# Performance work log

Hardware: AMD Instinct MI355X
Metric: run time of the kernel (lower is better)

Reference implementation:

```python
import jax, jax.numpy as jnp
import numpy as np

HIDDEN = 1024
HEADS = 16
HEAD_DIM = HIDDEN // HEADS

def setup_inputs() -> dict:
    key = jax.random.key(0)
    ks = jax.random.split(key, 11)
    B, T, D = 2, 2048, HIDDEN
    s = 1.0 / np.sqrt(D)
    return {
        "query": jax.random.normal(ks[0], (B, T, D), jnp.float32),
        "key": jax.random.normal(ks[1], (B, T, D), jnp.float32),
        "value": jax.random.normal(ks[2], (B, T, D), jnp.float32),
        "Wq": jax.random.normal(ks[3], (D, D), jnp.float32) * s,
        "bq": jnp.zeros((D,), jnp.float32),
        "Wk": jax.random.normal(ks[4], (D, D), jnp.float32) * s,
        "bk": jnp.zeros((D,), jnp.float32),
        "Wv": jax.random.normal(ks[5], (D, D), jnp.float32) * s,
        "bv": jnp.zeros((D,), jnp.float32),
        "Wo": jax.random.normal(ks[6], (D, D), jnp.float32) * s,
        "bo": jnp.zeros((D,), jnp.float32),
    }

def reference(query, key, value, Wq, bq, Wk, bk, Wv, bv, Wo, bo):
    B, Tq, D = query.shape
    Tk = key.shape[1]
    H, Hd = HEADS, HEAD_DIM
    # projections -> [B, H, T, Hd]
    Q = (query @ Wq + bq).reshape(B, Tq, H, Hd).transpose(0, 2, 1, 3)
    K = (key @ Wk + bk).reshape(B, Tk, H, Hd).transpose(0, 2, 1, 3)
    V = (value @ Wv + bv).reshape(B, Tk, H, Hd).transpose(0, 2, 1, 3)
    scale = jnp.sqrt(jnp.asarray(Hd, Q.dtype))
    scores = jnp.einsum('bhqd,bhkd->bhqk', Q, K) / scale  # [B,H,Tq,Tk]
    causal = jnp.triu(jnp.ones((Tq, Tk), bool), k=1)
    scores = jnp.where(causal[None, None], jnp.asarray(-jnp.inf, scores.dtype), scores)
    attn = jax.nn.softmax(scores, axis=-1)
    out = jnp.einsum('bhqk,bhkd->bhqd', attn, V)  # [B,H,Tq,Hd]
    out = out.transpose(0, 2, 1, 3).reshape(B, Tq, D)
    return out @ Wo + bo
```

## Files before the change

### kernel.cpp

```cpp
#include <hip/hip_runtime.h>
#include <hip/hip_bf16.h>


typedef __bf16 bf16_t;
typedef __bf16 bf16x8 __attribute__((ext_vector_type(8)));
typedef float f32x4 __attribute__((ext_vector_type(4)));
typedef float f32x16 __attribute__((ext_vector_type(16)));
typedef unsigned int u32;
typedef unsigned int u32x2v __attribute__((ext_vector_type(2)));
typedef unsigned int u32x4v __attribute__((ext_vector_type(4)));

#define D_MODEL 1024
#define SEQ_T   2048
#define NHEAD   16
#define HDIM    64
#define M_ROWS  4096
#define MEGA    (1024 * 1024)

__device__ __forceinline__ void gl2lds16(const void* g, void* l) {
    __builtin_amdgcn_global_load_lds((const __attribute__((address_space(1))) u32*)g,
                                     (__attribute__((address_space(3))) u32*)l, 16, 0, 0);
}

__device__ __forceinline__ u32 pk2(float a, float b) {
    unsigned short x = __builtin_bit_cast(unsigned short, (bf16_t)a);
    unsigned short y = __builtin_bit_cast(unsigned short, (bf16_t)b);
    return (u32)x | ((u32)y << 16);
}

__global__ __launch_bounds__(256) void prep(
    const float* __restrict__ Wq, const float* __restrict__ Wk,
    const float* __restrict__ Wv, const float* __restrict__ Wo,
    const float* __restrict__ Xq, const float* __restrict__ Xk, const float* __restrict__ Xv,
    bf16_t* __restrict__ Wqt, bf16_t* __restrict__ Wkt,
    bf16_t* __restrict__ Wvt, bf16_t* __restrict__ Wot,
    bf16_t* __restrict__ Xb)
{
    int blk = blockIdx.x, tid = threadIdx.x;
    if (blk < 4096) {
        int wi = blk >> 10, t = blk & 1023;
        int n0 = (t & 31) * 32, k0 = (t >> 5) * 32;
        const float* W = wi == 0 ? Wq : (wi == 1 ? Wk : (wi == 2 ? Wv : Wo));
        bf16_t* Wt = wi == 0 ? Wqt : (wi == 1 ? Wkt : (wi == 2 ? Wvt : Wot));
        __shared__ float tile[32][33];
        int tx = tid & 31, ty = tid >> 5;
#pragma unroll
        for (int i = 0; i < 32; i += 8)
            tile[ty + i][tx] = W[(k0 + ty + i) * D_MODEL + n0 + tx];
        __syncthreads();
#pragma unroll
        for (int i = 0; i < 32; i += 8)
            Wt[(size_t)(n0 + ty + i) * D_MODEL + k0 + tx] = (bf16_t)tile[tx][ty + i];
    } else {
        int b2 = blk - 4096;
        int xi = b2 >> 10;
        const float* X = xi == 0 ? Xq : (xi == 1 ? Xk : Xv);
        bf16_t* XB = Xb + (size_t)xi * M_ROWS * D_MODEL;
        size_t base = (size_t)(b2 & 1023) * 4096 + tid * 16;
        const float4* xp = (const float4*)(X + base);
        float4 a0 = xp[0], a1 = xp[1], a2 = xp[2], a3 = xp[3];
        bf16x8 o0, o1;
        o0[0] = (bf16_t)a0.x; o0[1] = (bf16_t)a0.y; o0[2] = (bf16_t)a0.z; o0[3] = (bf16_t)a0.w;
        o0[4] = (bf16_t)a1.x; o0[5] = (bf16_t)a1.y; o0[6] = (bf16_t)a1.z; o0[7] = (bf16_t)a1.w;
        o1[0] = (bf16_t)a2.x; o1[1] = (bf16_t)a2.y; o1[2] = (bf16_t)a2.z; o1[3] = (bf16_t)a2.w;
        o1[4] = (bf16_t)a3.x; o1[5] = (bf16_t)a3.y; o1[6] = (bf16_t)a3.z; o1[7] = (bf16_t)a3.w;
        *(bf16x8*)(XB + base) = o0;
        *(bf16x8*)(XB + base + 8) = o1;
    }
}

template <bool PRECAST>
__global__ __launch_bounds__(256) void proj_fused(
    const float* __restrict__ Xq, const float* __restrict__ Xk, const float* __restrict__ Xv,
    const bf16_t* __restrict__ Xb,
    const bf16_t* __restrict__ Wqt, const bf16_t* __restrict__ Wkt, const bf16_t* __restrict__ Wvt,
    const float* __restrict__ bq, const float* __restrict__ bk, const float* __restrict__ bv,
    bf16_t* __restrict__ Qh, bf16_t* __restrict__ Kh, bf16_t* __restrict__ Vt)
{
    __shared__ bf16_t Ab[128 * 64];
    __shared__ bf16_t Bb[128 * 64];
    int tid = threadIdx.x;
    int w = tid >> 6, lane = tid & 63, lo16 = lane & 15, quad = lane >> 4;
    int m0 = blockIdx.x * 128;
    int proj = blockIdx.y >> 3;
    int n0 = (blockIdx.y & 7) * 128;
    const float*  X    = proj == 0 ? Xq  : (proj == 1 ? Xk  : Xv);
    const bf16_t* XB   = Xb + (size_t)proj * M_ROWS * D_MODEL;
    const bf16_t* Wt   = proj == 0 ? Wqt : (proj == 1 ? Wkt : Wvt);
    const float*  bias = proj == 0 ? bq  : (proj == 1 ? bk  : bv);
    int wm = (w >> 1) * 64, wn = (w & 1) * 64;

    f32x4 acc[4][4];
#pragma unroll
    for (int i = 0; i < 4; i++)
#pragma unroll
        for (int j = 0; j < 4; j++) acc[i][j] = (f32x4){0.f, 0.f, 0.f, 0.f};

    for (int k0 = 0; k0 < D_MODEL; k0 += 64) {
        __syncthreads();
#pragma unroll
        for (int p = 0; p < 4; p++) {
            int idx = p * 256 + tid;
            int row = idx >> 3, cp = idx & 7, cl = (cp - row) & 7;
            if (PRECAST) {
                gl2lds16(XB + (size_t)(m0 + row) * D_MODEL + k0 + cl * 8, Ab + idx * 8);
            } else {
                const float* as = X + (size_t)(m0 + row) * D_MODEL + k0 + cl * 8;
                float4 a0 = *(const float4*)as, a1 = *(const float4*)(as + 4);
                bf16x8 av;
                av[0] = (bf16_t)a0.x; av[1] = (bf16_t)a0.y; av[2] = (bf16_t)a0.z; av[3] = (bf16_t)a0.w;
                av[4] = (bf16_t)a1.x; av[5] = (bf16_t)a1.y; av[6] = (bf16_t)a1.z; av[7] = (bf16_t)a1.w;
                *(bf16x8*)(Ab + idx * 8) = av;
            }
            gl2lds16(Wt + (size_t)(n0 + row) * D_MODEL + k0 + cl * 8, Bb + idx * 8);
        }
        __syncthreads();
#pragma unroll
        for (int kk = 0; kk < 2; kk++) {
            bf16x8 af[4], bfr[4];
#pragma unroll
            for (int i = 0; i < 4; i++) {
                int row = wm + i * 16 + lo16;
                af[i] = *(bf16x8*)(Ab + row * 64 + ((4 * kk + quad + row) & 7) * 8);
            }
#pragma unroll
            for (int j = 0; j < 4; j++) {
                int row = wn + j * 16 + lo16;
                bfr[j] = *(bf16x8*)(Bb + row * 64 + ((4 * kk + quad + row) & 7) * 8);
            }
#pragma unroll
            for (int i = 0; i < 4; i++)
#pragma unroll
                for (int j = 0; j < 4; j++)
                    acc[i][j] = __builtin_amdgcn_mfma_f32_16x16x32_bf16(af[i], bfr[j], acc[i][j], 0, 0, 0);
        }
    }

    float qscale = proj == 0 ? 0.1803368801111244f : 1.0f;
#pragma unroll
    for (int j = 0; j < 4; j++) {
        int col = n0 + wn + j * 16 + lo16;
        float bv2 = bias[col];
        int h = col >> 6, hd = col & 63;
#pragma unroll
        for (int i = 0; i < 4; i++) {
#pragma unroll
            for (int r = 0; r < 4; r++) {
                int m = m0 + wm + i * 16 + quad * 4 + r;
                int b = m >> 11, t = m & 2047;
                bf16_t val = (bf16_t)((acc[i][j][r] + bv2) * qscale);
                if (proj == 2)
                    Vt[(((size_t)(b * NHEAD + h) * HDIM + hd) * SEQ_T) + t] = val;
                else if (proj == 1)
                    Kh[(((size_t)(b * NHEAD + h) * SEQ_T + t) * HDIM) + hd] = val;
                else
                    Qh[(((size_t)(b * NHEAD + h) * SEQ_T + t) * HDIM) + hd] = val;
            }
        }
    }
}

__global__ __launch_bounds__(128, 2) void flash_attn(const bf16_t* __restrict__ Qh,
                                                     const bf16_t* __restrict__ Kh,
                                                     const bf16_t* __restrict__ Vt,
                                                     bf16_t* __restrict__ Ob) {
    int blk = blockIdx.x;
    int bh = blk & 31;
    int s5 = blk >> 5;
    int seg = s5 >> 3, o = s5 & 7;
    int j = seg == 0 ? 31 - o : (seg == 1 ? 16 + o : (seg == 2 ? 15 - o : o));
    int tid = threadIdx.x;
    int w = tid >> 6, lane = tid & 63;
    int l32 = lane & 31, hi = lane >> 5;
    int qbase = j * 64 + w * 32;

    __shared__ bf16_t KL[2][64 * 64];
    __shared__ bf16_t VL[2][64 * 64];

    const bf16_t* Qp = Qh + (size_t)bh * SEQ_T * HDIM;
    const bf16_t* Kp = Kh + (size_t)bh * SEQ_T * HDIM;
    const bf16_t* Vp = Vt + (size_t)bh * HDIM * SEQ_T;

    bf16x8 qf[4];
    {
        const bf16_t* qr = Qp + (size_t)(qbase + l32) * HDIM;
#pragma unroll
        for (int kd = 0; kd < 4; kd++)
            qf[kd] = *(const bf16x8*)(qr + kd * 16 + hi * 8);
    }

    bf16x8 ones;
#pragma unroll
    for (int i = 0; i < 8; i++) ones[i] = (bf16_t)1.0f;

    f32x16 oacc[2], lacc;
#pragma unroll
    for (int r = 0; r < 16; r++) { oacc[0][r] = 0.f; oacc[1][r] = 0.f; lacc[r] = 0.f; }

    int nkt = j + 1;

#pragma unroll
    for (int p = 0; p < 4; p++) {
        int idx = p * 128 + tid;
        int row = idx >> 3, cp = idx & 7, cl = (cp - row) & 7;
        gl2lds16(Kp + (size_t)row * HDIM + cl * 8, KL[0] + idx * 8);
        gl2lds16(Vp + (size_t)row * SEQ_T + cl * 8, VL[0] + idx * 8);
    }

    for (int kt = 0; kt < nkt; kt++) {
        int cur = kt & 1;
        __syncthreads();

        if (kt + 1 < nkt) {
#pragma unroll
            for (int p = 0; p < 4; p++) {
                int idx = p * 128 + tid;
                int row = idx >> 3, cp = idx & 7, cl = (cp - row) & 7;
                gl2lds16(Kp + (size_t)((kt + 1) * 64 + row) * HDIM + cl * 8, KL[cur ^ 1] + idx * 8);
                gl2lds16(Vp + (size_t)row * SEQ_T + (kt + 1) * 64 + cl * 8, VL[cur ^ 1] + idx * 8);
            }
        }
        const bf16_t* KLc = KL[cur];
        const bf16_t* VLc = VL[cur];

        f32x16 sacc[2];
#pragma unroll
        for (int r = 0; r < 16; r++) { sacc[0][r] = 0.f; sacc[1][r] = 0.f; }
#pragma unroll
        for (int ks = 0; ks < 2; ks++) {
            int key = l32 + 32 * ks;
#pragma unroll
            for (int kd = 0; kd < 4; kd++) {
                bf16x8 kf = *(const bf16x8*)(KLc + key * 64 + ((2 * kd + hi + key) & 7) * 8);
                sacc[ks] = __builtin_amdgcn_mfma_f32_32x32x16_bf16(kf, qf[kd], sacc[ks], 0, 0, 0);
            }
        }

        bool diag = (kt == nkt - 1);
        int qg = qbase + l32;
#pragma unroll
        for (int ks = 0; ks < 2; ks++)
#pragma unroll
            for (int r = 0; r < 16; r++) {
                float e = exp2f(sacc[ks][r]);
                if (diag) {
                    int key = kt * 64 + ks * 32 + (r & 3) + 8 * (r >> 2) + 4 * hi;
                    e = (key <= qg) ? e : 0.f;
                }
                sacc[ks][r] = e;
            }

        bf16x8 pf[4];
#pragma unroll
        for (int t = 0; t < 4; t++) {
            const int ks = t >> 1, bb = (t & 1) * 8;
            u32 A1 = pk2(sacc[ks][bb + 0], sacc[ks][bb + 1]);
            u32 A2 = pk2(sacc[ks][bb + 2], sacc[ks][bb + 3]);
            u32 C1 = pk2(sacc[ks][bb + 4], sacc[ks][bb + 5]);
            u32 C2 = pk2(sacc[ks][bb + 6], sacc[ks][bb + 7]);
            u32x2v s1 = __builtin_amdgcn_permlane32_swap(A1, C1, false, false);
            u32x2v s2 = __builtin_amdgcn_permlane32_swap(A2, C2, false, false);
            u32x4v wv; wv[0] = s1[0]; wv[1] = s2[0]; wv[2] = s1[1]; wv[3] = s2[1];
            pf[t] = __builtin_bit_cast(bf16x8, wv);
            lacc = __builtin_amdgcn_mfma_f32_32x32x16_bf16(pf[t], ones, lacc, 0, 0, 0);
        }

#pragma unroll
        for (int dt = 0; dt < 2; dt++) {
            int d = l32 + 32 * dt;
#pragma unroll
            for (int t = 0; t < 4; t++) {
                bf16x8 vf = *(const bf16x8*)(VLc + d * 64 + ((2 * t + hi + d) & 7) * 8);
                oacc[dt] = __builtin_amdgcn_mfma_f32_32x32x16_bf16(pf[t], vf, oacc[dt], 0, 0, 0);
            }
        }
    }

    int b = bh >> 4, h = bh & 15;
    float inv[16];
#pragma unroll
    for (int r = 0; r < 16; r++) inv[r] = 1.0f / lacc[r];
#pragma unroll
    for (int dt = 0; dt < 2; dt++)
#pragma unroll
        for (int r = 0; r < 16; r++) {
            int q = qbase + (r & 3) + 8 * (r >> 2) + 4 * hi;
            int d = l32 + 32 * dt;
            Ob[((size_t)b * SEQ_T + q) * D_MODEL + h * HDIM + d] = (bf16_t)(oacc[dt][r] * inv[r]);
        }
}

__global__ __launch_bounds__(256) void out_gemm(const bf16_t* __restrict__ A,
                                                const bf16_t* __restrict__ Wt,
                                                const float* __restrict__ bias,
                                                float* __restrict__ out) {
    __shared__ bf16_t Ab[128 * 64];
    __shared__ bf16_t Bb[128 * 64];
    int tid = threadIdx.x;
    int w = tid >> 6, lane = tid & 63, lo16 = lane & 15, quad = lane >> 4;
    int m0 = blockIdx.x * 128;
    int n0 = blockIdx.y * 128;
    int wm = (w >> 1) * 64, wn = (w & 1) * 64;

    f32x4 acc[4][4];
#pragma unroll
    for (int i = 0; i < 4; i++)
#pragma unroll
        for (int j = 0; j < 4; j++) acc[i][j] = (f32x4){0.f, 0.f, 0.f, 0.f};

    for (int k0 = 0; k0 < D_MODEL; k0 += 64) {
        __syncthreads();
#pragma unroll
        for (int p = 0; p < 4; p++) {
            int idx = p * 256 + tid;
            int row = idx >> 3, cp = idx & 7, cl = (cp - row) & 7;
            gl2lds16(A  + (size_t)(m0 + row) * D_MODEL + k0 + cl * 8, Ab + idx * 8);
            gl2lds16(Wt + (size_t)(n0 + row) * D_MODEL + k0 + cl * 8, Bb + idx * 8);
        }
        __syncthreads();
#pragma unroll
        for (int kk = 0; kk < 2; kk++) {
            bf16x8 af[4], bfr[4];
#pragma unroll
            for (int i = 0; i < 4; i++) {
                int row = wm + i * 16 + lo16;
                af[i] = *(bf16x8*)(Ab + row * 64 + ((4 * kk + quad + row) & 7) * 8);
            }
#pragma unroll
            for (int j = 0; j < 4; j++) {
                int row = wn + j * 16 + lo16;
                bfr[j] = *(bf16x8*)(Bb + row * 64 + ((4 * kk + quad + row) & 7) * 8);
            }
#pragma unroll
            for (int i = 0; i < 4; i++)
#pragma unroll
                for (int j = 0; j < 4; j++)
                    acc[i][j] = __builtin_amdgcn_mfma_f32_16x16x32_bf16(af[i], bfr[j], acc[i][j], 0, 0, 0);
        }
    }

#pragma unroll
    for (int j = 0; j < 4; j++) {
        int col = n0 + wn + j * 16 + lo16;
        float bv2 = bias[col];
#pragma unroll
        for (int i = 0; i < 4; i++)
#pragma unroll
            for (int r = 0; r < 4; r++) {
                int m = m0 + wm + i * 16 + quad * 4 + r;
                out[(size_t)m * D_MODEL + col] = acc[i][j][r] + bv2;
            }
    }
}

extern "C" void kernel_launch(void* const* d_in, const int* in_sizes, int n_in,
                              void* d_out, int out_size, void* d_ws, size_t ws_size,
                              hipStream_t stream) {
    const float* q  = (const float*)d_in[0];
    const float* k  = (const float*)d_in[1];
    const float* v  = (const float*)d_in[2];
    const float* Wq = (const float*)d_in[3];
    const float* bq = (const float*)d_in[4];
    const float* Wk = (const float*)d_in[5];
    const float* bk = (const float*)d_in[6];
    const float* Wv = (const float*)d_in[7];
    const float* bv = (const float*)d_in[8];
    const float* Wo = (const float*)d_in[9];
    const float* bo = (const float*)d_in[10];
    float* out = (float*)d_out;

    bf16_t* Wqt = (bf16_t*)d_ws;
    bf16_t* Wkt = Wqt + (size_t)MEGA;
    bf16_t* Wvt = Wkt + (size_t)MEGA;
    bf16_t* Wot = Wvt + (size_t)MEGA;
    bf16_t* Qh  = Wot + (size_t)MEGA;
    bf16_t* Kh  = Qh  + (size_t)M_ROWS * D_MODEL;
    bf16_t* Vt  = Kh  + (size_t)M_ROWS * D_MODEL;
    bf16_t* Xb  = Vt  + (size_t)M_ROWS * D_MODEL;
    bf16_t* Ob  = Xb;

    bool precast = ws_size >= (size_t)(4 * MEGA + 3 * M_ROWS * D_MODEL + 3 * M_ROWS * D_MODEL) * sizeof(bf16_t);

    int prep_blocks = precast ? 4096 + 3 * 1024 : 4096;
    prep<<<prep_blocks, 256, 0, stream>>>(Wq, Wk, Wv, Wo, q, k, v, Wqt, Wkt, Wvt, Wot, Xb);

    dim3 pg(M_ROWS / 128, 24);
    if (precast)
        proj_fused<true><<<pg, 256, 0, stream>>>(q, k, v, Xb, Wqt, Wkt, Wvt, bq, bk, bv, Qh, Kh, Vt);
    else
        proj_fused<false><<<pg, 256, 0, stream>>>(q, k, v, Xb, Wqt, Wkt, Wvt, bq, bk, bv, Qh, Kh, Vt);

    flash_attn<<<32 * 32, 128, 0, stream>>>(Qh, Kh, Vt, Ob);

    dim3 og(M_ROWS / 128, D_MODEL / 128);
    out_gemm<<<og, 256, 0, stream>>>(Ob, Wot, bo, out);
}
```

Baseline: 245.2 us.

## Split long causal attention rows across two blocks and add combine kernel

Flash attention now reads a constant job table that splits query tiles 17–31 into two KV ranges. The two partial blocks write unnormalized outputs and row sums to a float workspace, and a new combine kernel adds the partials and normalizes. The aim is to balance the triangular causal workload across more blocks and shorten the tail. Separately, both GEMMs switch from a K-tile of 64 to 32 and drop the LDS swizzle, which halves shared memory but doubles the number of barrier steps and may cause bank conflicts. The new partial buffer sits past the checked workspace size and adds an extra kernel launch and global traffic.

```diff
diff --git a/kernel.cpp b/kernel.cpp
--- a/kernel.cpp
+++ b/kernel.cpp
@@ -3,6 +3,7 @@
 
 
 typedef __bf16 bf16_t;
+typedef __bf16 bf16x4 __attribute__((ext_vector_type(4)));
 typedef __bf16 bf16x8 __attribute__((ext_vector_type(8)));
 typedef float f32x4 __attribute__((ext_vector_type(4)));
 typedef float f32x16 __attribute__((ext_vector_type(16)));
@@ -27,6 +28,21 @@
     unsigned short y = __builtin_bit_cast(unsigned short, (bf16_t)b);
     return (u32)x | ((u32)y << 16);
 }
+
+#define JOB(j, k0, n) ((j) | ((k0) << 8) | ((n) << 16))
+__device__ __constant__ int JOBS[47] = {
+    JOB(16,0,17),
+    JOB(15,0,16), JOB(30,0,16), JOB(31,0,16), JOB(31,16,16),
+    JOB(14,0,15), JOB(28,0,15), JOB(29,0,15), JOB(29,15,15), JOB(30,16,15),
+    JOB(13,0,14), JOB(26,0,14), JOB(27,0,14), JOB(27,14,14), JOB(28,15,14),
+    JOB(12,0,13), JOB(24,0,13), JOB(25,0,13), JOB(25,13,13), JOB(26,14,13),
+    JOB(11,0,12), JOB(22,0,12), JOB(23,0,12), JOB(23,12,12), JOB(24,13,12),
+    JOB(10,0,11), JOB(20,0,11), JOB(21,0,11), JOB(21,11,11), JOB(22,12,11),
+    JOB( 9,0,10), JOB(18,0,10), JOB(19,0,10), JOB(19,10,10), JOB(20,11,10),
+    JOB( 8,0, 9), JOB(17,0, 9), JOB(17,9, 9), JOB(18,10, 9),
+    JOB( 7,0, 8), JOB( 6,0, 7), JOB( 5,0, 6), JOB( 4,0, 5),
+    JOB( 3,0, 4), JOB( 2,0, 3), JOB( 1,0, 2), JOB( 0,0, 1)
+};
 
 __global__ __launch_bounds__(256) void prep(
     const float* __restrict__ Wq, const float* __restrict__ Wk,
@@ -77,8 +93,8 @@
     const float* __restrict__ bq, const float* __restrict__ bk, const float* __restrict__ bv,
     bf16_t* __restrict__ Qh, bf16_t* __restrict__ Kh, bf16_t* __restrict__ Vt)
 {
-    __shared__ bf16_t Ab[128 * 64];
-    __shared__ bf16_t Bb[128 * 64];
+    __shared__ bf16_t Ab[128 * 32];
+    __shared__ bf16_t Bb[128 * 32];
     int tid = threadIdx.x;
     int w = tid >> 6, lane = tid & 63, lo16 = lane & 15, quad = lane >> 4;
     int m0 = blockIdx.x * 128;
@@ -96,44 +112,37 @@
 #pragma unroll
         for (int j = 0; j < 4; j++) acc[i][j] = (f32x4){0.f, 0.f, 0.f, 0.f};
 
-    for (int k0 = 0; k0 < D_MODEL; k0 += 64) {
-        __syncthreads();
-#pragma unroll
-        for (int p = 0; p < 4; p++) {
+    for (int k0 = 0; k0 < D_MODEL; k0 += 32) {
+        __syncthreads();
+#pragma unroll
+        for (int p = 0; p < 2; p++) {
             int idx = p * 256 + tid;
-            int row = idx >> 3, cp = idx & 7, cl = (cp - row) & 7;
+            int row = idx >> 2, ch = (idx & 3) * 8;
             if (PRECAST) {
-                gl2lds16(XB + (size_t)(m0 + row) * D_MODEL + k0 + cl * 8, Ab + idx * 8);
+                gl2lds16(XB + (size_t)(m0 + row) * D_MODEL + k0 + ch, Ab + idx * 8);
             } else {
-                const float* as = X + (size_t)(m0 + row) * D_MODEL + k0 + cl * 8;
+                const float* as = X + (size_t)(m0 + row) * D_MODEL + k0 + ch;
                 float4 a0 = *(const float4*)as, a1 = *(const float4*)(as + 4);
                 bf16x8 av;
                 av[0] = (bf16_t)a0.x; av[1] = (bf16_t)a0.y; av[2] = (bf16_t)a0.z; av[3] = (bf16_t)a0.w;
                 av[4] = (bf16_t)a1.x; av[5] = (bf16_t)a1.y; av[6] = (bf16_t)a1.z; av[7] = (bf16_t)a1.w;
                 *(bf16x8*)(Ab + idx * 8) = av;
             }
-            gl2lds16(Wt + (size_t)(n0 + row) * D_MODEL + k0 + cl * 8, Bb + idx * 8);
-        }
-        __syncthreads();
-#pragma unroll
-        for (int kk = 0; kk < 2; kk++) {
-            bf16x8 af[4], bfr[4];
-#pragma unroll
-            for (int i = 0; i < 4; i++) {
-                int row = wm + i * 16 + lo16;
-                af[i] = *(bf16x8*)(Ab + row * 64 + ((4 * kk + quad + row) & 7) * 8);
-            }
-#pragma unroll
-            for (int j = 0; j < 4; j++) {
-                int row = wn + j * 16 + lo16;
-                bfr[j] = *(bf16x8*)(Bb + row * 64 + ((4 * kk + quad + row) & 7) * 8);
-            }
-#pragma unroll
-            for (int i = 0; i < 4; i++)
-#pragma unroll
-                for (int j = 0; j < 4; j++)
-                    acc[i][j] = __builtin_amdgcn_mfma_f32_16x16x32_bf16(af[i], bfr[j], acc[i][j], 0, 0, 0);
-        }
+            gl2lds16(Wt + (size_t)(n0 + row) * D_MODEL + k0 + ch, Bb + idx * 8);
+        }
+        __syncthreads();
+        bf16x8 af[4], bfr[4];
+#pragma unroll
+        for (int i = 0; i < 4; i++)
+            af[i] = *(bf16x8*)(Ab + (wm + i * 16 + lo16) * 32 + quad * 8);
+#pragma unroll
+        for (int j = 0; j < 4; j++)
+            bfr[j] = *(bf16x8*)(Bb + (wn + j * 16 + lo16) * 32 + quad * 8);
+#pragma unroll
+        for (int i = 0; i < 4; i++)
+#pragma unroll
+            for (int j = 0; j < 4; j++)
+                acc[i][j] = __builtin_amdgcn_mfma_f32_16x16x32_bf16(af[i], bfr[j], acc[i][j], 0, 0, 0);
     }
 
     float qscale = proj == 0 ? 0.1803368801111244f : 1.0f;
@@ -163,12 +172,12 @@
 __global__ __launch_bounds__(128, 2) void flash_attn(const bf16_t* __restrict__ Qh,
                                                      const bf16_t* __restrict__ Kh,
                                                      const bf16_t* __restrict__ Vt,
-                                                     bf16_t* __restrict__ Ob) {
+                                                     bf16_t* __restrict__ Ob,
+                                                     float* __restrict__ Pw) {
     int blk = blockIdx.x;
     int bh = blk & 31;
-    int s5 = blk >> 5;
-    int seg = s5 >> 3, o = s5 & 7;
-    int j = seg == 0 ? 31 - o : (seg == 1 ? 16 + o : (seg == 2 ? 15 - o : o));
+    int enc = JOBS[blk >> 5];
+    int j = enc & 255, kt0 = (enc >> 8) & 255, nkt = (enc >> 16) & 255;
     int tid = threadIdx.x;
     int w = tid >> 6, lane = tid & 63;
     int l32 = lane & 31, hi = lane >> 5;
@@ -197,21 +206,20 @@
 #pragma unroll
     for (int r = 0; r < 16; r++) { oacc[0][r] = 0.f; oacc[1][r] = 0.f; lacc[r] = 0.f; }
 
-    int nkt = j + 1;
-
 #pragma unroll
     for (int p = 0; p < 4; p++) {
         int idx = p * 128 + tid;
         int row = idx >> 3, cp = idx & 7, cl = (cp - row) & 7;
-        gl2lds16(Kp + (size_t)row * HDIM + cl * 8, KL[0] + idx * 8);
-        gl2lds16(Vp + (size_t)row * SEQ_T + cl * 8, VL[0] + idx * 8);
-    }
-
-    for (int kt = 0; kt < nkt; kt++) {
-        int cur = kt & 1;
-        __syncthreads();
-
-        if (kt + 1 < nkt) {
+        gl2lds16(Kp + (size_t)(kt0 * 64 + row) * HDIM + cl * 8, KL[0] + idx * 8);
+        gl2lds16(Vp + (size_t)row * SEQ_T + kt0 * 64 + cl * 8, VL[0] + idx * 8);
+    }
+
+    for (int it = 0; it < nkt; it++) {
+        int kt = kt0 + it;
+        int cur = it & 1;
+        __syncthreads();
+
+        if (it + 1 < nkt) {
 #pragma unroll
             for (int p = 0; p < 4; p++) {
                 int idx = p * 128 + tid;
@@ -236,7 +244,7 @@
             }
         }
 
-        bool diag = (kt == nkt - 1);
+        bool diag = (kt == j);
         int qg = qbase + l32;
 #pragma unroll
         for (int ks = 0; ks < 2; ks++)
@@ -276,26 +284,71 @@
         }
     }
 
+    if (j >= 17) {
+        int c = kt0 ? 1 : 0;
+        float* slot = Pw + (size_t)((bh * 15 + (j - 17)) * 2 + c) * 4160;
+#pragma unroll
+        for (int dt = 0; dt < 2; dt++)
+#pragma unroll
+            for (int r = 0; r < 16; r++) {
+                int qrow = w * 32 + (r & 3) + 8 * (r >> 2) + 4 * hi;
+                slot[qrow * 64 + l32 + 32 * dt] = oacc[dt][r];
+            }
+        if (l32 == 0) {
+#pragma unroll
+            for (int r = 0; r < 16; r++)
+                slot[4096 + w * 32 + (r & 3) + 8 * (r >> 2) + 4 * hi] = lacc[r];
+        }
+    } else {
+        int b = bh >> 4, h = bh & 15;
+        float inv[16];
+#pragma unroll
+        for (int r = 0; r < 16; r++) inv[r] = 1.0f / lacc[r];
+#pragma unroll
+        for (int dt = 0; dt < 2; dt++)
+#pragma unroll
+            for (int r = 0; r < 16; r++) {
+                int q = qbase + (r & 3) + 8 * (r >> 2) + 4 * hi;
+                int d = l32 + 32 * dt;
+                Ob[((size_t)b * SEQ_T + q) * D_MODEL + h * HDIM + d] = (bf16_t)(oacc[dt][r] * inv[r]);
+            }
+    }
+}
+
+__global__ __launch_bounds__(256) void combine(const float* __restrict__ Pw,
+                                               bf16_t* __restrict__ Ob) {
+    int blk = blockIdx.x;
+    int bh = blk / 15, jj = blk % 15;
+    int j = jj + 17;
     int b = bh >> 4, h = bh & 15;
-    float inv[16];
-#pragma unroll
-    for (int r = 0; r < 16; r++) inv[r] = 1.0f / lacc[r];
-#pragma unroll
-    for (int dt = 0; dt < 2; dt++)
-#pragma unroll
-        for (int r = 0; r < 16; r++) {
-            int q = qbase + (r & 3) + 8 * (r >> 2) + 4 * hi;
-            int d = l32 + 32 * dt;
-            Ob[((size_t)b * SEQ_T + q) * D_MODEL + h * HDIM + d] = (bf16_t)(oacc[dt][r] * inv[r]);
-        }
+    const float* s0 = Pw + (size_t)blk * 8320;
+    const float* s1 = s0 + 4160;
+    __shared__ float linv[64];
+    int tid = threadIdx.x;
+    if (tid < 64) linv[tid] = 1.0f / (s0[4096 + tid] + s1[4096 + tid]);
+    __syncthreads();
+#pragma unroll
+    for (int i = 0; i < 4; i++) {
+        int e = i * 1024 + tid * 4;
+        f32x4 a = *(const f32x4*)(s0 + e);
+        f32x4 c = *(const f32x4*)(s1 + e);
+        int q = e >> 6, d = e & 63;
+        float il = linv[q];
+        bf16x4 o;
+        o[0] = (bf16_t)((a[0] + c[0]) * il);
+        o[1] = (bf16_t)((a[1] + c[1]) * il);
+        o[2] = (bf16_t)((a[2] + c[2]) * il);
+        o[3] = (bf16_t)((a[3] + c[3]) * il);
+        *(bf16x4*)(Ob + ((size_t)b * SEQ_T + j * 64 + q) * D_MODEL + h * HDIM + d) = o;
+    }
 }
 
 __global__ __launch_bounds__(256) void out_gemm(const bf16_t* __restrict__ A,
                                                 const bf16_t* __restrict__ Wt,
                                                 const float* __restrict__ bias,
                                                 float* __restrict__ out) {
-    __shared__ bf16_t Ab[128 * 64];
-    __shared__ bf16_t Bb[128 * 64];
+    __shared__ bf16_t Ab[128 * 32];
+    __shared__ bf16_t Bb[128 * 32];
     int tid = threadIdx.x;
     int w = tid >> 6, lane = tid & 63, lo16 = lane & 15, quad = lane >> 4;
     int m0 = blockIdx.x * 128;
@@ -308,35 +361,28 @@
 #pragma unroll
         for (int j = 0; j < 4; j++) acc[i][j] = (f32x4){0.f, 0.f, 0.f, 0.f};
 
-    for (int k0 = 0; k0 < D_MODEL; k0 += 64) {
-        __syncthreads();
-#pragma unroll
-        for (int p = 0; p < 4; p++) {
+    for (int k0 = 0; k0 < D_MODEL; k0 += 32) {
+        __syncthreads();
+#pragma unroll
+        for (int p = 0; p < 2; p++) {
             int idx = p * 256 + tid;
-            int row = idx >> 3, cp = idx & 7, cl = (cp - row) & 7;
-            gl2lds16(A  + (size_t)(m0 + row) * D_MODEL + k0 + cl * 8, Ab + idx * 8);
-            gl2lds16(Wt + (size_t)(n0 + row) * D_MODEL + k0 + cl * 8, Bb + idx * 8);
-        }
-        __syncthreads();
-#pragma unroll
-        for (int kk = 0; kk < 2; kk++) {
-            bf16x8 af[4], bfr[4];
-#pragma unroll
-            for (int i = 0; i < 4; i++) {
-                int row = wm + i * 16 + lo16;
-                af[i] = *(bf16x8*)(Ab + row * 64 + ((4 * kk + quad + row) & 7) * 8);
-            }
-#pragma unroll
-            for (int j = 0; j < 4; j++) {
-                int row = wn + j * 16 + lo16;
-                bfr[j] = *(bf16x8*)(Bb + row * 64 + ((4 * kk + quad + row) & 7) * 8);
-            }
-#pragma unroll
-            for (int i = 0; i < 4; i++)
-#pragma unroll
-                for (int j = 0; j < 4; j++)
-                    acc[i][j] = __builtin_amdgcn_mfma_f32_16x16x32_bf16(af[i], bfr[j], acc[i][j], 0, 0, 0);
-        }
+            int row = idx >> 2, ch = (idx & 3) * 8;
+            gl2lds16(A  + (size_t)(m0 + row) * D_MODEL + k0 + ch, Ab + idx * 8);
+            gl2lds16(Wt + (size_t)(n0 + row) * D_MODEL + k0 + ch, Bb + idx * 8);
+        }
+        __syncthreads();
+        bf16x8 af[4], bfr[4];
+#pragma unroll
+        for (int i = 0; i < 4; i++)
+            af[i] = *(bf16x8*)(Ab + (wm + i * 16 + lo16) * 32 + quad * 8);
+#pragma unroll
+        for (int j = 0; j < 4; j++)
+            bfr[j] = *(bf16x8*)(Bb + (wn + j * 16 + lo16) * 32 + quad * 8);
+#pragma unroll
+        for (int i = 0; i < 4; i++)
+#pragma unroll
+            for (int j = 0; j < 4; j++)
+                acc[i][j] = __builtin_amdgcn_mfma_f32_16x16x32_bf16(af[i], bfr[j], acc[i][j], 0, 0, 0);
     }
 
 #pragma unroll
@@ -378,6 +424,7 @@
     bf16_t* Vt  = Kh  + (size_t)M_ROWS * D_MODEL;
     bf16_t* Xb  = Vt  + (size_t)M_ROWS * D_MODEL;
     bf16_t* Ob  = Xb;
+    float*  Pw  = (float*)(Xb + (size_t)M_ROWS * D_MODEL);
 
     bool precast = ws_size >= (size_t)(4 * MEGA + 3 * M_ROWS * D_MODEL + 3 * M_ROWS * D_MODEL) * sizeof(bf16_t);
 
@@ -390,7 +437,8 @@
     else
         proj_fused<false><<<pg, 256, 0, stream>>>(q, k, v, Xb, Wqt, Wkt, Wvt, bq, bk, bv, Qh, Kh, Vt);
 
-    flash_attn<<<32 * 32, 128, 0, stream>>>(Qh, Kh, Vt, Ob);
+    flash_attn<<<47 * 32, 128, 0, stream>>>(Qh, Kh, Vt, Ob, Pw);
+    combine<<<32 * 15, 256, 0, stream>>>(Pw, Ob);
 
     dim3 og(M_ROWS / 128, D_MODEL / 128);
     out_gemm<<<og, 256, 0, stream>>>(Ob, Wot, bo, out);
```

Measured after the change: 238.1 us. 1.03x faster.
